# Performance work log

Hardware: AMD Instinct MI355X
Metric: run time of the kernel (lower is better)

## Reference

```python
import jax, jax.numpy as jnp
import numpy as np

B, T, C = 2, 2048, 1024
H = 16
DH = C // H  # 64
EPS = 1e-5


def setup_inputs() -> dict:
    key = jax.random.key(0)
    ks = jax.random.split(key, 12)
    s = lambda k, shape, fan: jax.random.normal(k, shape, jnp.float32) / np.sqrt(fan)
    return {
        'x': jax.random.normal(ks[0], (B, T, C), jnp.float32),
        'wq': s(ks[1], (H, C, DH), C),
        'wk': s(ks[2], (H, C, DH), C),
        'wv': s(ks[3], (H, C, DH), C),
        'w_proj': s(ks[4], (C, C), C),
        'b_proj': jnp.zeros((C,), jnp.float32),
        'g_ln1': jnp.ones((C,), jnp.float32),
        'b_ln1': jnp.zeros((C,), jnp.float32),
        'g_ln2': jnp.ones((C,), jnp.float32),
        'b_ln2': jnp.zeros((C,), jnp.float32),
        'w_ff1': s(ks[5], (C, 4 * C), C),
        'b_ff1': jnp.zeros((4 * C,), jnp.float32),
        'w_ff2': s(ks[6], (4 * C, C), 4 * C),
        'b_ff2': jnp.zeros((C,), jnp.float32),
    }


def _layernorm(x, g, b):
    mu = jnp.mean(x, axis=-1, keepdims=True)
    var = jnp.mean(jnp.square(x - mu), axis=-1, keepdims=True)
    return (x - mu) * jax.lax.rsqrt(var + EPS) * g + b


def _attention(x, wq, wk, wv, w_proj, b_proj):
    # per-head projections, batched over heads: [B,T,C] x [H,C,Dh] -> [B,H,T,Dh]
    q = jnp.einsum('btc,hcd->bhtd', x, wq)
    k = jnp.einsum('btc,hcd->bhtd', x, wk)
    v = jnp.einsum('btc,hcd->bhtd', x, wv)
    scores = jnp.einsum('bhtd,bhsd->bhts', q, k) / np.sqrt(DH).astype(np.float32)
    t = x.shape[1]
    causal = jnp.tril(jnp.ones((t, t), bool))
    scores = jnp.where(causal, scores, -jnp.inf)
    w = jax.nn.softmax(scores, axis=-1)
    out = jnp.einsum('bhts,bhsd->bhtd', w, v)  # [B,H,T,Dh]
    # concat heads (head order matches torch cat over head list)
    out = out.transpose(0, 2, 1, 3).reshape(x.shape[0], t, C)
    return out @ w_proj + b_proj


def reference(x, wq, wk, wv, w_proj, b_proj, g_ln1, b_ln1, g_ln2, b_ln2, w_ff1, b_ff1, w_ff2, b_ff2):
    x = x + _attention(_layernorm(x, g_ln1, b_ln1), wq, wk, wv, w_proj, b_proj)
    h = _layernorm(x, g_ln2, b_ln2)
    ff = jax.nn.relu(h @ w_ff1 + b_ff1) @ w_ff2 + b_ff2
    return x + ff
```

## Files before the change

### kernel.cpp

```cpp
#include <hip/hip_runtime.h>

#define DEV __device__ __forceinline__

typedef __attribute__((ext_vector_type(4))) float f32x4;
typedef __attribute__((ext_vector_type(8))) short short8;
typedef __attribute__((ext_vector_type(8))) __bf16 bf16x8;

DEV unsigned short f2bf(float f) {
  __bf16 h = (__bf16)f;
  return __builtin_bit_cast(unsigned short, h);
}
DEV unsigned pack2(float a, float b) {
  return (unsigned)f2bf(a) | ((unsigned)f2bf(b) << 16);
}
DEV bf16x8 ld_bf8(const unsigned short* p) {
  short8 v = *(const short8*)p;
  return __builtin_bit_cast(bf16x8, v);
}
DEV f32x4 MFMA(bf16x8 a, bf16x8 b, f32x4 c) {
  return __builtin_amdgcn_mfma_f32_16x16x32_bf16(a, b, c, 0, 0, 0);
}

typedef const __attribute__((address_space(1))) void GV;
typedef __attribute__((address_space(3))) void LV;
DEV void gl_lds16(const void* g, void* l) {
  __builtin_amdgcn_global_load_lds((GV*)g, (LV*)l, 16, 0, 0);
}

DEV void xcd_decode(int gx, int& bx, int& by) {
  const int nwg = gridDim.x, bid = blockIdx.x;
  const int cpx = nwg >> 3;
  const int swz = (bid & 7) * cpx + (bid >> 3);
  by = swz / gx;
  bx = swz % gx;
}

__global__ void __launch_bounds__(256) ln_fused(
    const float* __restrict__ x, const float* __restrict__ g,
    const float* __restrict__ b, unsigned short* __restrict__ y)
{
  const int row = blockIdx.x, tid = threadIdx.x;
  const float4 xv = ((const float4*)(x + (size_t)row * 1024))[tid];
  float s  = xv.x + xv.y + xv.z + xv.w;
  float s2 = xv.x * xv.x + xv.y * xv.y + xv.z * xv.z + xv.w * xv.w;
#pragma unroll
  for (int o = 32; o > 0; o >>= 1) { s += __shfl_down(s, o); s2 += __shfl_down(s2, o); }
  __shared__ float ps[4], ps2[4];
  if ((tid & 63) == 0) { ps[tid >> 6] = s; ps2[tid >> 6] = s2; }
  __syncthreads();
  float S  = ps[0] + ps[1] + ps[2] + ps[3];
  float S2 = ps2[0] + ps2[1] + ps2[2] + ps2[3];
  float mu = S * (1.f / 1024.f);
  float rs = rsqrtf(S2 * (1.f / 1024.f) - mu * mu + 1e-5f);
  const float4 gv = ((const float4*)g)[tid];
  const float4 bv = ((const float4*)b)[tid];
  uint2 r;
  r.x = pack2((xv.x - mu) * rs * gv.x + bv.x, (xv.y - mu) * rs * gv.y + bv.y);
  r.y = pack2((xv.z - mu) * rs * gv.z + bv.z, (xv.w - mu) * rs * gv.w + bv.w);
  ((uint2*)(y + (size_t)row * 1024))[tid] = r;
}

__global__ void __launch_bounds__(256) transp_f2b(
    const float* __restrict__ src, unsigned short* __restrict__ dst, int R, int C)
{
  __shared__ float t[64][65];
  const int c0 = blockIdx.x * 64, r0 = blockIdx.y * 64;
  const int tx = threadIdx.x & 63, tq = threadIdx.x >> 6;
#pragma unroll
  for (int i = 0; i < 16; i++) {
    int r = tq * 16 + i;
    t[r][tx] = src[(size_t)(r0 + r) * C + c0 + tx];
  }
  __syncthreads();
#pragma unroll
  for (int i = 0; i < 16; i++) {
    int c = tq * 16 + i;
    dst[(size_t)(c0 + c) * R + r0 + tx] = f2bf(t[tx][c]);
  }
}

__global__ void __launch_bounds__(256) qkv_transp(
    const float* __restrict__ wq, const float* __restrict__ wk,
    const float* __restrict__ wv, unsigned short* __restrict__ dst)
{
  __shared__ float t[64][65];
  const int c0 = blockIdx.x * 64, h = blockIdx.y, z = blockIdx.z;
  const float* w = (z == 0 ? wq : z == 1 ? wk : wv) + (size_t)h * 1024 * 64;
  const int tx = threadIdx.x & 63, tq = threadIdx.x >> 6;
#pragma unroll
  for (int i = 0; i < 16; i++) {
    int c = tq * 16 + i;
    t[c][tx] = w[(size_t)(c0 + c) * 64 + tx];
  }
  __syncthreads();
  unsigned short* drow = dst + (size_t)(z * 1024 + h * 64) * 1024 + c0;
#pragma unroll
  for (int i = 0; i < 16; i++) {
    int d = tq * 16 + i;
    drow[(size_t)d * 1024 + tx] = f2bf(t[tx][d]);
  }
}

__global__ void __launch_bounds__(256) v_transp(
    const unsigned short* __restrict__ qkv, unsigned short* __restrict__ vt)
{
  __shared__ unsigned s[64][65];
  const int t0 = blockIdx.x * 64, h = blockIdx.y, b = blockIdx.z;
  const int tx = threadIdx.x & 63, tq = threadIdx.x >> 6;
#pragma unroll
  for (int i = 0; i < 16; i++) {
    int tr = tq * 16 + i;
    s[tr][tx] = qkv[(size_t)(b * 2048 + t0 + tr) * 3072 + 2048 + h * 64 + tx];
  }
  __syncthreads();
  unsigned short* vb = vt + (size_t)((b * 16 + h) * 64) * 2048 + t0;
#pragma unroll
  for (int i = 0; i < 16; i++) {
    int d = tq * 16 + i;
    vb[(size_t)d * 2048 + tx] = (unsigned short)s[tx][d];
  }
}

template<int BIAS, int RELU, int RES, int OBF>
__global__ void __launch_bounds__(256) gemm_bt(
    const unsigned short* __restrict__ A, const unsigned short* __restrict__ Bt,
    const float* __restrict__ bias, const float* __restrict__ res,
    void* __restrict__ out, int M, int N, int K, int gx)
{
  __shared__ unsigned short As[2][128 * 32];
  __shared__ unsigned short Bs[2][128 * 32];
  int bx, by;
  xcd_decode(gx, bx, by);
  const int tid = threadIdx.x;
  const int wid = tid >> 6, lane = tid & 63;
  const int lg = lane >> 4, lr = lane & 15;
  const int m0 = by * 128, n0 = bx * 128;
  const int wr = (wid >> 1) * 64, wc = (wid & 1) * 64;

  const int srow = tid >> 2;
  const int scs = (tid & 3) ^ (srow & 3);
  const unsigned short* ga = A + (size_t)(m0 + srow) * K + scs * 8;
  const unsigned short* gb = Bt + (size_t)(n0 + srow) * K + scs * 8;
  const int ca = (lg ^ (lr & 3)) * 8;

  f32x4 acc[4][4] = {};

  auto stage = [&](int buf, int k0) {
    char* asb = (char*)&As[buf][0] + wid * 1024;
    char* bsb = (char*)&Bs[buf][0] + wid * 1024;
    gl_lds16(ga + k0, asb);
    gl_lds16(ga + k0 + (size_t)64 * K, asb + 4096);
    gl_lds16(gb + k0, bsb);
    gl_lds16(gb + k0 + (size_t)64 * K, bsb + 4096);
  };

  stage(0, 0);
  int cur = 0;
  for (int k0 = 0; k0 < K; k0 += 32) {
    __syncthreads();
    if (k0 + 32 < K) stage(cur ^ 1, k0 + 32);
    bf16x8 a[4], b[4];
#pragma unroll
    for (int m = 0; m < 4; m++) a[m] = ld_bf8(&As[cur][(wr + m * 16 + lr) * 32 + ca]);
#pragma unroll
    for (int n = 0; n < 4; n++) b[n] = ld_bf8(&Bs[cur][(wc + n * 16 + lr) * 32 + ca]);
#pragma unroll
    for (int m = 0; m < 4; m++)
#pragma unroll
      for (int n = 0; n < 4; n++)
        acc[m][n] = MFMA(a[m], b[n], acc[m][n]);
    cur ^= 1;
  }

#pragma unroll
  for (int m = 0; m < 4; m++) {
    const int row0 = m0 + wr + m * 16 + lg * 4;
#pragma unroll
    for (int n = 0; n < 4; n++) {
      const int col = n0 + wc + n * 16 + lr;
      const float bv = BIAS ? bias[col] : 0.f;
#pragma unroll
      for (int r = 0; r < 4; r++) {
        const size_t off = (size_t)(row0 + r) * N + col;
        float v = acc[m][n][r] + bv;
        if (RES) v += res[off];
        if (RELU) v = v > 0.f ? v : 0.f;
        if (OBF) ((unsigned short*)out)[off] = f2bf(v);
        else     ((float*)out)[off] = v;
      }
    }
  }
}

template<int BIAS, int RELU, int RES, int OBF>
__global__ void __launch_bounds__(256) gemm_bt64(
    const unsigned short* __restrict__ A, const unsigned short* __restrict__ Bt,
    const float* __restrict__ bias, const float* __restrict__ res,
    void* __restrict__ out, int M, int N, int K, int gx)
{
  __shared__ unsigned short As[2][64 * 64];
  __shared__ unsigned short Bs[2][128 * 64];
  int bx, by;
  xcd_decode(gx, bx, by);
  const int tid = threadIdx.x;
  const int wid = tid >> 6, lane = tid & 63;
  const int lg = lane >> 4, lr = lane & 15;
  const int m0 = by * 64, n0 = bx * 128;
  const int wr = (wid >> 1) * 32, wc = (wid & 1) * 64;

  const int srow = tid >> 3;
  const int scs = (tid & 7) ^ (srow & 7);
  const unsigned short* ga = A + (size_t)(m0 + srow) * K + scs * 8;
  const unsigned short* gb = Bt + (size_t)(n0 + srow) * K + scs * 8;
  const int lxs = lr & 7;

  f32x4 acc[2][4] = {};

  auto stage = [&](int buf, int k0) {
    char* asb = (char*)&As[buf][0] + wid * 1024;
    char* bsb = (char*)&Bs[buf][0] + wid * 1024;
    gl_lds16(ga + k0, asb);
    gl_lds16(ga + k0 + (size_t)32 * K, asb + 4096);
    gl_lds16(gb + k0, bsb);
    gl_lds16(gb + k0 + (size_t)32 * K, bsb + 4096);
    gl_lds16(gb + k0 + (size_t)64 * K, bsb + 8192);
    gl_lds16(gb + k0 + (size_t)96 * K, bsb + 12288);
  };

  stage(0, 0);
  int cur = 0;
  for (int k0 = 0; k0 < K; k0 += 64) {
    __syncthreads();
    if (k0 + 64 < K) stage(cur ^ 1, k0 + 64);
#pragma unroll
    for (int kk = 0; kk < 2; kk++) {
      const int cb = kk * 4;
      bf16x8 a[2], b[4];
#pragma unroll
      for (int m = 0; m < 2; m++)
        a[m] = ld_bf8(&As[cur][(wr + m * 16 + lr) * 64 + ((cb + lg) ^ lxs) * 8]);
#pragma unroll
      for (int n = 0; n < 4; n++)
        b[n] = ld_bf8(&Bs[cur][(wc + n * 16 + lr) * 64 + ((cb + lg) ^ lxs) * 8]);
#pragma unroll
      for (int m = 0; m < 2; m++)
#pragma unroll
        for (int n = 0; n < 4; n++)
          acc[m][n] = MFMA(a[m], b[n], acc[m][n]);
    }
    cur ^= 1;
  }

#pragma unroll
  for (int m = 0; m < 2; m++) {
    const int row0 = m0 + wr + m * 16 + lg * 4;
#pragma unroll
    for (int n = 0; n < 4; n++) {
      const int col = n0 + wc + n * 16 + lr;
      const float bv = BIAS ? bias[col] : 0.f;
#pragma unroll
      for (int r = 0; r < 4; r++) {
        const size_t off = (size_t)(row0 + r) * N + col;
        float v = acc[m][n][r] + bv;
        if (RES) v += res[off];
        if (RELU) v = v > 0.f ? v : 0.f;
        if (OBF) ((unsigned short*)out)[off] = f2bf(v);
        else     ((float*)out)[off] = v;
      }
    }
  }
}

__global__ void __launch_bounds__(256) attn_fwd(
    const unsigned short* __restrict__ qkv, const unsigned short* __restrict__ vt,
    unsigned short* __restrict__ out)
{
  __shared__ unsigned short Ks[2][64 * 64];
  __shared__ unsigned short Vs[2][64 * 64];
  __shared__ unsigned short P[4][16][72];

  int j, bh;
  xcd_decode(16, j, bh);
  const int b = bh >> 4, h = bh & 15;
  const int tid = threadIdx.x, wid = tid >> 6, lane = tid & 63;
  const int lg = lane >> 4, lr = lane & 15;

  const int tA = j, tB = 31 - j;
  const int nkt = tB + 1;
  const float C2 = 0.18033688f;
  const float THRRAW = 44.3614f;

  const unsigned short* kbase = qkv + (size_t)(b * 2048) * 3072 + 1024 + h * 64;
  const unsigned short* vbase = vt + (size_t)(bh * 64) * 2048;

  const int sr = tid >> 3;
  const int sc = tid & 7;
  const int c0 = sc ^ (sr & 7);

  auto stage = [&](int buf, int kt) {
    const int kv0 = kt * 64;
    char* kd = (char*)&Ks[buf][0] + wid * 1024;
    char* vd = (char*)&Vs[buf][0] + wid * 1024;
    gl_lds16(kbase + (size_t)(kv0 + sr) * 3072 + c0 * 8, kd);
    gl_lds16(kbase + (size_t)(kv0 + 32 + sr) * 3072 + c0 * 8, kd + 4096);
    gl_lds16(vbase + (size_t)sr * 2048 + kv0 + c0 * 8, vd);
    gl_lds16(vbase + (size_t)(32 + sr) * 2048 + kv0 + c0 * 8, vd + 4096);
  };

  auto process = [&](int kt, int qt, const bf16x8& qf0, const bf16x8& qf1,
                     f32x4 (&o)[4], float& m, float& l, int buf) {
    const int kv0 = kt * 64;
    const int qg = qt * 64 + wid * 16 + lr;
    const unsigned short* Kb = &Ks[buf][0];
    const unsigned short* Vb = &Vs[buf][0];
    f32x4 s[4] = {};
    __builtin_amdgcn_s_setprio(1);
#pragma unroll
    for (int f = 0; f < 4; f++) {
      const int row = f * 16 + lr;
      const int rc = row & 7;
      s[f] = MFMA(ld_bf8(Kb + row * 64 + (lg ^ rc) * 8), qf0, s[f]);
      s[f] = MFMA(ld_bf8(Kb + row * 64 + ((lg | 4) ^ rc) * 8), qf1, s[f]);
    }
    __builtin_amdgcn_s_setprio(0);
    float p[16];
    float mt = -1e30f;
    const bool diag = (kt == qt);
#pragma unroll
    for (int f = 0; f < 4; f++)
#pragma unroll
      for (int r = 0; r < 4; r++) {
        float sv = s[f][r];
        if (diag) {
          const int kv = kv0 + f * 16 + lg * 4 + r;
          sv = (kv <= qg) ? sv : -1e30f;
        }
        p[f * 4 + r] = sv;
        mt = fmaxf(mt, sv);
      }
    mt = fmaxf(mt, __shfl_xor(mt, 16));
    mt = fmaxf(mt, __shfl_xor(mt, 32));
    if (!__all(mt - m <= THRRAW)) {
      const float mnew = fmaxf(m, mt);
      const float sf = exp2f(C2 * (m - mnew));
      l *= sf;
#pragma unroll
      for (int df = 0; df < 4; df++) o[df] *= sf;
      m = mnew;
    }
    const float cm = C2 * m;
    float ps = 0.f;
#pragma unroll
    for (int i = 0; i < 16; i++) {
      p[i] = exp2f(fmaf(p[i], C2, -cm));
      ps += p[i];
    }
    ps += __shfl_xor(ps, 16);
    ps += __shfl_xor(ps, 32);
    l += ps;
    unsigned short* Pr = &P[wid][lr][0];
#pragma unroll
    for (int f = 0; f < 4; f++) {
      *(unsigned*)(Pr + f * 16 + lg * 4)     = pack2(p[f * 4 + 0], p[f * 4 + 1]);
      *(unsigned*)(Pr + f * 16 + lg * 4 + 2) = pack2(p[f * 4 + 2], p[f * 4 + 3]);
    }
    const bf16x8 pf0 = ld_bf8(Pr + lg * 8);
    const bf16x8 pf1 = ld_bf8(Pr + 32 + lg * 8);
    __builtin_amdgcn_s_setprio(1);
#pragma unroll
    for (int df = 0; df < 4; df++) {
      const int row = df * 16 + lr;
      const int rc = row & 7;
      o[df] = MFMA(ld_bf8(Vb + row * 64 + (lg ^ rc) * 8), pf0, o[df]);
      o[df] = MFMA(ld_bf8(Vb + row * 64 + ((lg | 4) ^ rc) * 8), pf1, o[df]);
    }
    __builtin_amdgcn_s_setprio(0);
  };

  const unsigned short* qb = qkv + (size_t)(b * 2048) * 3072 + h * 64;
  const int qrA = tA * 64 + wid * 16 + lr;
  const int qrB = tB * 64 + wid * 16 + lr;
  const bf16x8 qA0 = ld_bf8(qb + (size_t)qrA * 3072 + lg * 8);
  const bf16x8 qA1 = ld_bf8(qb + (size_t)qrA * 3072 + 32 + lg * 8);
  const bf16x8 qB0 = ld_bf8(qb + (size_t)qrB * 3072 + lg * 8);
  const bf16x8 qB1 = ld_bf8(qb + (size_t)qrB * 3072 + 32 + lg * 8);

  f32x4 oA[4] = {}, oB[4] = {};
  float mA = -1e30f, lA = 0.f, mB = -1e30f, lB = 0.f;

  stage(0, 0);
  __syncthreads();
  for (int kt = 0; kt < nkt; kt++) {
    const int buf = kt & 1;
    if (kt + 1 < nkt) stage(buf ^ 1, kt + 1);
    if (kt <= tA) process(kt, tA, qA0, qA1, oA, mA, lA, buf);
    process(kt, tB, qB0, qB1, oB, mB, lB, buf);
    __syncthreads();
  }

  const float invA = 1.f / lA, invB = 1.f / lB;
  {
    const int qg = tA * 64 + wid * 16 + lr;
    unsigned* orow = (unsigned*)(out + (size_t)(b * 2048 + qg) * 1024 + h * 64 + lg * 4);
#pragma unroll
    for (int df = 0; df < 4; df++) {
      orow[df * 8 + 0] = pack2(oA[df][0] * invA, oA[df][1] * invA);
      orow[df * 8 + 1] = pack2(oA[df][2] * invA, oA[df][3] * invA);
    }
  }
  {
    const int qg = tB * 64 + wid * 16 + lr;
    unsigned* orow = (unsigned*)(out + (size_t)(b * 2048 + qg) * 1024 + h * 64 + lg * 4);
#pragma unroll
    for (int df = 0; df < 4; df++) {
      orow[df * 8 + 0] = pack2(oB[df][0] * invB, oB[df][1] * invB);
      orow[df * 8 + 1] = pack2(oB[df][2] * invB, oB[df][3] * invB);
    }
  }
}

extern "C" void kernel_launch(void* const* d_in, const int* in_sizes, int n_in,
                              void* d_out, int out_size, void* d_ws, size_t ws_size,
                              hipStream_t stream)
{
  const float* x     = (const float*)d_in[0];
  const float* wq    = (const float*)d_in[1];
  const float* wk    = (const float*)d_in[2];
  const float* wv    = (const float*)d_in[3];
  const float* wproj = (const float*)d_in[4];
  const float* bproj = (const float*)d_in[5];
  const float* gln1  = (const float*)d_in[6];
  const float* bln1  = (const float*)d_in[7];
  const float* gln2  = (const float*)d_in[8];
  const float* bln2  = (const float*)d_in[9];
  const float* wff1  = (const float*)d_in[10];
  const float* bff1  = (const float*)d_in[11];
  const float* wff2  = (const float*)d_in[12];
  const float* bff2  = (const float*)d_in[13];

  char* ws = (char*)d_ws;
  const size_t MB = 1u << 20;
  float*          x2    = (float*)         (ws + 0 * MB);
  unsigned short* hbuf  = (unsigned short*)(ws + 16 * MB);
  unsigned short* xn1   = (unsigned short*)(ws + 24 * MB);
  unsigned short* attn  = (unsigned short*)(ws + 24 * MB);
  unsigned short* qkvb  = (unsigned short*)(ws + 32 * MB);
  unsigned short* vtb   = (unsigned short*)(ws + 56 * MB);
  unsigned short* a1    = (unsigned short*)(ws + 32 * MB);
  unsigned short* wqkvT = (unsigned short*)(ws + 64 * MB);
  unsigned short* wprojT= (unsigned short*)(ws + 70 * MB);
  unsigned short* wff1T = (unsigned short*)(ws + 72 * MB);
  unsigned short* wff2T = (unsigned short*)(ws + 80 * MB);

  qkv_transp<<<dim3(16, 16, 3), 256, 0, stream>>>(wq, wk, wv, wqkvT);
  transp_f2b<<<dim3(16, 16), 256, 0, stream>>>(wproj, wprojT, 1024, 1024);
  transp_f2b<<<dim3(64, 16), 256, 0, stream>>>(wff1, wff1T, 1024, 4096);
  transp_f2b<<<dim3(16, 64), 256, 0, stream>>>(wff2, wff2T, 4096, 1024);

  ln_fused<<<4096, 256, 0, stream>>>(x, gln1, bln1, xn1);
  gemm_bt<0, 0, 0, 1><<<768, 256, 0, stream>>>(
      xn1, wqkvT, nullptr, nullptr, qkvb, 4096, 3072, 1024, 24);
  v_transp<<<dim3(32, 16, 2), 256, 0, stream>>>(qkvb, vtb);
  attn_fwd<<<512, 256, 0, stream>>>(qkvb, vtb, attn);
  gemm_bt64<1, 0, 1, 0><<<512, 256, 0, stream>>>(
      attn, wprojT, bproj, x, x2, 4096, 1024, 1024, 8);
  ln_fused<<<4096, 256, 0, stream>>>(x2, gln2, bln2, hbuf);
  gemm_bt<1, 1, 0, 1><<<1024, 256, 0, stream>>>(
      hbuf, wff1T, bff1, nullptr, a1, 4096, 4096, 1024, 32);
  gemm_bt64<1, 0, 1, 0><<<512, 256, 0, stream>>>(
      a1, wff2T, bff2, x2, (float*)d_out, 4096, 1024, 4096, 8);
}
```

Measured before the change: 253.0 us.

## Split attention into one query tile per block and shrink N-narrow GEMM tiles

The attention kernel no longer pairs two query tiles per block for causal load balancing. It now launches 1024 blocks, each handling one query tile, with a swizzled block index that schedules the longest tiles first. The two narrow-N GEMMs (output projection and FFN2) use 64x64 tiles instead of 64x128, doubling the block count. The aim is more blocks in flight on the many CUs, at the cost of less data reuse per block and uneven per-block work in attention.

Result: slower. 259.9 us (+2.7%).

```diff
diff --git a/kernel.cpp b/kernel.cpp
--- a/kernel.cpp
+++ b/kernel.cpp
@@ -193,20 +193,20 @@
 }
 
 template<int BIAS, int RELU, int RES, int OBF>
-__global__ void __launch_bounds__(256) gemm_bt64(
+__global__ void __launch_bounds__(256) gemm_64(
     const unsigned short* __restrict__ A, const unsigned short* __restrict__ Bt,
     const float* __restrict__ bias, const float* __restrict__ res,
     void* __restrict__ out, int M, int N, int K, int gx)
 {
   __shared__ unsigned short As[2][64 * 64];
-  __shared__ unsigned short Bs[2][128 * 64];
+  __shared__ unsigned short Bs[2][64 * 64];
   int bx, by;
   xcd_decode(gx, bx, by);
   const int tid = threadIdx.x;
   const int wid = tid >> 6, lane = tid & 63;
   const int lg = lane >> 4, lr = lane & 15;
-  const int m0 = by * 64, n0 = bx * 128;
-  const int wr = (wid >> 1) * 32, wc = (wid & 1) * 64;
+  const int m0 = by * 64, n0 = bx * 64;
+  const int wr = (wid >> 1) * 32, wc = (wid & 1) * 32;
 
   const int srow = tid >> 3;
   const int scs = (tid & 7) ^ (srow & 7);
@@ -214,7 +214,7 @@
   const unsigned short* gb = Bt + (size_t)(n0 + srow) * K + scs * 8;
   const int lxs = lr & 7;
 
-  f32x4 acc[2][4] = {};
+  f32x4 acc[2][2] = {};
 
   auto stage = [&](int buf, int k0) {
     char* asb = (char*)&As[buf][0] + wid * 1024;
@@ -223,8 +223,6 @@
     gl_lds16(ga + k0 + (size_t)32 * K, asb + 4096);
     gl_lds16(gb + k0, bsb);
     gl_lds16(gb + k0 + (size_t)32 * K, bsb + 4096);
-    gl_lds16(gb + k0 + (size_t)64 * K, bsb + 8192);
-    gl_lds16(gb + k0 + (size_t)96 * K, bsb + 12288);
   };
 
   stage(0, 0);
@@ -235,17 +233,17 @@
 #pragma unroll
     for (int kk = 0; kk < 2; kk++) {
       const int cb = kk * 4;
-      bf16x8 a[2], b[4];
+      bf16x8 a[2], b[2];
 #pragma unroll
       for (int m = 0; m < 2; m++)
         a[m] = ld_bf8(&As[cur][(wr + m * 16 + lr) * 64 + ((cb + lg) ^ lxs) * 8]);
 #pragma unroll
-      for (int n = 0; n < 4; n++)
+      for (int n = 0; n < 2; n++)
         b[n] = ld_bf8(&Bs[cur][(wc + n * 16 + lr) * 64 + ((cb + lg) ^ lxs) * 8]);
 #pragma unroll
       for (int m = 0; m < 2; m++)
 #pragma unroll
-        for (int n = 0; n < 4; n++)
+        for (int n = 0; n < 2; n++)
           acc[m][n] = MFMA(a[m], b[n], acc[m][n]);
     }
     cur ^= 1;
@@ -255,7 +253,7 @@
   for (int m = 0; m < 2; m++) {
     const int row0 = m0 + wr + m * 16 + lg * 4;
 #pragma unroll
-    for (int n = 0; n < 4; n++) {
+    for (int n = 0; n < 2; n++) {
       const int col = n0 + wc + n * 16 + lr;
       const float bv = BIAS ? bias[col] : 0.f;
 #pragma unroll
@@ -279,14 +277,15 @@
   __shared__ unsigned short Vs[2][64 * 64];
   __shared__ unsigned short P[4][16][72];
 
-  int j, bh;
-  xcd_decode(16, j, bh);
+  const int bid = blockIdx.x;
+  const int swz = (bid & 7) * 128 + (bid >> 3);
+  const int bh = swz >> 5;
+  const int qt = 31 - (swz & 31);
   const int b = bh >> 4, h = bh & 15;
   const int tid = threadIdx.x, wid = tid >> 6, lane = tid & 63;
   const int lg = lane >> 4, lr = lane & 15;
 
-  const int tA = j, tB = 31 - j;
-  const int nkt = tB + 1;
+  const int nkt = qt + 1;
   const float C2 = 0.18033688f;
   const float THRRAW = 44.3614f;
 
@@ -307,10 +306,21 @@
     gl_lds16(vbase + (size_t)(32 + sr) * 2048 + kv0 + c0 * 8, vd + 4096);
   };
 
-  auto process = [&](int kt, int qt, const bf16x8& qf0, const bf16x8& qf1,
-                     f32x4 (&o)[4], float& m, float& l, int buf) {
+  const unsigned short* qb = qkv + (size_t)(b * 2048) * 3072 + h * 64;
+  const int qg = qt * 64 + wid * 16 + lr;
+  const bf16x8 qf0 = ld_bf8(qb + (size_t)qg * 3072 + lg * 8);
+  const bf16x8 qf1 = ld_bf8(qb + (size_t)qg * 3072 + 32 + lg * 8);
+
+  f32x4 o[4] = {};
+  float m = -1e30f, l = 0.f;
+
+  stage(0, 0);
+  __syncthreads();
+  for (int kt = 0; kt < nkt; kt++) {
+    const int buf = kt & 1;
+    if (kt + 1 < nkt) stage(buf ^ 1, kt + 1);
+
     const int kv0 = kt * 64;
-    const int qg = qt * 64 + wid * 16 + lr;
     const unsigned short* Kb = &Ks[buf][0];
     const unsigned short* Vb = &Vs[buf][0];
     f32x4 s[4] = {};
@@ -375,47 +385,15 @@
       o[df] = MFMA(ld_bf8(Vb + row * 64 + ((lg | 4) ^ rc) * 8), pf1, o[df]);
     }
     __builtin_amdgcn_s_setprio(0);
-  };
-
-  const unsigned short* qb = qkv + (size_t)(b * 2048) * 3072 + h * 64;
-  const int qrA = tA * 64 + wid * 16 + lr;
-  const int qrB = tB * 64 + wid * 16 + lr;
-  const bf16x8 qA0 = ld_bf8(qb + (size_t)qrA * 3072 + lg * 8);
-  const bf16x8 qA1 = ld_bf8(qb + (size_t)qrA * 3072 + 32 + lg * 8);
-  const bf16x8 qB0 = ld_bf8(qb + (size_t)qrB * 3072 + lg * 8);
-  const bf16x8 qB1 = ld_bf8(qb + (size_t)qrB * 3072 + 32 + lg * 8);
-
-  f32x4 oA[4] = {}, oB[4] = {};
-  float mA = -1e30f, lA = 0.f, mB = -1e30f, lB = 0.f;
-
-  stage(0, 0);
-  __syncthreads();
-  for (int kt = 0; kt < nkt; kt++) {
-    const int buf = kt & 1;
-    if (kt + 1 < nkt) stage(buf ^ 1, kt + 1);
-    if (kt <= tA) process(kt, tA, qA0, qA1, oA, mA, lA, buf);
-    process(kt, tB, qB0, qB1, oB, mB, lB, buf);
     __syncthreads();
   }
 
-  const float invA = 1.f / lA, invB = 1.f / lB;
-  {
-    const int qg = tA * 64 + wid * 16 + lr;
-    unsigned* orow = (unsigned*)(out + (size_t)(b * 2048 + qg) * 1024 + h * 64 + lg * 4);
-#pragma unroll
-    for (int df = 0; df < 4; df++) {
-      orow[df * 8 + 0] = pack2(oA[df][0] * invA, oA[df][1] * invA);
-      orow[df * 8 + 1] = pack2(oA[df][2] * invA, oA[df][3] * invA);
-    }
-  }
-  {
-    const int qg = tB * 64 + wid * 16 + lr;
-    unsigned* orow = (unsigned*)(out + (size_t)(b * 2048 + qg) * 1024 + h * 64 + lg * 4);
-#pragma unroll
-    for (int df = 0; df < 4; df++) {
-      orow[df * 8 + 0] = pack2(oB[df][0] * invB, oB[df][1] * invB);
-      orow[df * 8 + 1] = pack2(oB[df][2] * invB, oB[df][3] * invB);
-    }
+  const float inv = 1.f / l;
+  unsigned* orow = (unsigned*)(out + (size_t)(b * 2048 + qg) * 1024 + h * 64 + lg * 4);
+#pragma unroll
+  for (int df = 0; df < 4; df++) {
+    orow[df * 8 + 0] = pack2(o[df][0] * inv, o[df][1] * inv);
+    orow[df * 8 + 1] = pack2(o[df][2] * inv, o[df][3] * inv);
   }
 }
 
@@ -461,12 +439,12 @@
   gemm_bt<0, 0, 0, 1><<<768, 256, 0, stream>>>(
       xn1, wqkvT, nullptr, nullptr, qkvb, 4096, 3072, 1024, 24);
   v_transp<<<dim3(32, 16, 2), 256, 0, stream>>>(qkvb, vtb);
-  attn_fwd<<<512, 256, 0, stream>>>(qkvb, vtb, attn);
-  gemm_bt64<1, 0, 1, 0><<<512, 256, 0, stream>>>(
-      attn, wprojT, bproj, x, x2, 4096, 1024, 1024, 8);
+  attn_fwd<<<1024, 256, 0, stream>>>(qkvb, vtb, attn);
+  gemm_64<1, 0, 1, 0><<<1024, 256, 0, stream>>>(
+      attn, wprojT, bproj, x, x2, 4096, 1024, 1024, 16);
   ln_fused<<<4096, 256, 0, stream>>>(x2, gln2, bln2, hbuf);
   gemm_bt<1, 1, 0, 1><<<1024, 256, 0, stream>>>(
       hbuf, wff1T, bff1, nullptr, a1, 4096, 4096, 1024, 32);
-  gemm_bt64<1, 0, 1, 0><<<512, 256, 0, stream>>>(
-      a1, wff2T, bff2, x2, (float*)d_out, 4096, 1024, 4096, 8);
-}
+  gemm_64<1, 0, 1, 0><<<1024, 256, 0, stream>>>(
+      a1, wff2T, bff2, x2, (float*)d_out, 4096, 1024, 4096, 16);
+}
```

## Use 64x64 GEMM tiles for N=1024 projections and stage 128 KV rows in attention

Applied to the files above, without the earlier changes.

The N=1024 GEMMs (output projection and FF2) switch from 64x128 to 64x64 tiles, doubling the grid to 1024 blocks so the GPU's CUs are better filled. Separately, the attention kernel now stages K/V in 128-row chunks and processes two 64-row tiles per barrier, halving the number of synchronisations per KV sweep. The trade-offs are lower per-block operand reuse in the GEMMs and twice the K/V shared memory in attention, which can reduce occupancy.

After: 247.1 us. -2.3%, faster.

```diff
diff --git a/kernel.cpp b/kernel.cpp
--- a/kernel.cpp
+++ b/kernel.cpp
@@ -193,20 +193,20 @@
 }
 
 template<int BIAS, int RELU, int RES, int OBF>
-__global__ void __launch_bounds__(256) gemm_bt64(
+__global__ void __launch_bounds__(256) gemm_64(
     const unsigned short* __restrict__ A, const unsigned short* __restrict__ Bt,
     const float* __restrict__ bias, const float* __restrict__ res,
     void* __restrict__ out, int M, int N, int K, int gx)
 {
   __shared__ unsigned short As[2][64 * 64];
-  __shared__ unsigned short Bs[2][128 * 64];
+  __shared__ unsigned short Bs[2][64 * 64];
   int bx, by;
   xcd_decode(gx, bx, by);
   const int tid = threadIdx.x;
   const int wid = tid >> 6, lane = tid & 63;
   const int lg = lane >> 4, lr = lane & 15;
-  const int m0 = by * 64, n0 = bx * 128;
-  const int wr = (wid >> 1) * 32, wc = (wid & 1) * 64;
+  const int m0 = by * 64, n0 = bx * 64;
+  const int wr = (wid >> 1) * 32, wc = (wid & 1) * 32;
 
   const int srow = tid >> 3;
   const int scs = (tid & 7) ^ (srow & 7);
@@ -214,7 +214,7 @@
   const unsigned short* gb = Bt + (size_t)(n0 + srow) * K + scs * 8;
   const int lxs = lr & 7;
 
-  f32x4 acc[2][4] = {};
+  f32x4 acc[2][2] = {};
 
   auto stage = [&](int buf, int k0) {
     char* asb = (char*)&As[buf][0] + wid * 1024;
@@ -223,8 +223,6 @@
     gl_lds16(ga + k0 + (size_t)32 * K, asb + 4096);
     gl_lds16(gb + k0, bsb);
     gl_lds16(gb + k0 + (size_t)32 * K, bsb + 4096);
-    gl_lds16(gb + k0 + (size_t)64 * K, bsb + 8192);
-    gl_lds16(gb + k0 + (size_t)96 * K, bsb + 12288);
   };
 
   stage(0, 0);
@@ -235,17 +233,17 @@
 #pragma unroll
     for (int kk = 0; kk < 2; kk++) {
       const int cb = kk * 4;
-      bf16x8 a[2], b[4];
+      bf16x8 a[2], b[2];
 #pragma unroll
       for (int m = 0; m < 2; m++)
         a[m] = ld_bf8(&As[cur][(wr + m * 16 + lr) * 64 + ((cb + lg) ^ lxs) * 8]);
 #pragma unroll
-      for (int n = 0; n < 4; n++)
+      for (int n = 0; n < 2; n++)
         b[n] = ld_bf8(&Bs[cur][(wc + n * 16 + lr) * 64 + ((cb + lg) ^ lxs) * 8]);
 #pragma unroll
       for (int m = 0; m < 2; m++)
 #pragma unroll
-        for (int n = 0; n < 4; n++)
+        for (int n = 0; n < 2; n++)
           acc[m][n] = MFMA(a[m], b[n], acc[m][n]);
     }
     cur ^= 1;
@@ -255,7 +253,7 @@
   for (int m = 0; m < 2; m++) {
     const int row0 = m0 + wr + m * 16 + lg * 4;
 #pragma unroll
-    for (int n = 0; n < 4; n++) {
+    for (int n = 0; n < 2; n++) {
       const int col = n0 + wc + n * 16 + lr;
       const float bv = BIAS ? bias[col] : 0.f;
 #pragma unroll
@@ -275,8 +273,8 @@
     const unsigned short* __restrict__ qkv, const unsigned short* __restrict__ vt,
     unsigned short* __restrict__ out)
 {
-  __shared__ unsigned short Ks[2][64 * 64];
-  __shared__ unsigned short Vs[2][64 * 64];
+  __shared__ unsigned short Ks[2][128 * 64];
+  __shared__ unsigned short Vs[2][128 * 64];
   __shared__ unsigned short P[4][16][72];
 
   int j, bh;
@@ -287,6 +285,7 @@
 
   const int tA = j, tB = 31 - j;
   const int nkt = tB + 1;
+  const int npair = (nkt + 1) >> 1;
   const float C2 = 0.18033688f;
   const float THRRAW = 44.3614f;
 
@@ -297,22 +296,26 @@
   const int sc = tid & 7;
   const int c0 = sc ^ (sr & 7);
 
-  auto stage = [&](int buf, int kt) {
-    const int kv0 = kt * 64;
+  auto stage = [&](int buf, int p) {
+    const int kv0 = p * 128;
     char* kd = (char*)&Ks[buf][0] + wid * 1024;
     char* vd = (char*)&Vs[buf][0] + wid * 1024;
     gl_lds16(kbase + (size_t)(kv0 + sr) * 3072 + c0 * 8, kd);
     gl_lds16(kbase + (size_t)(kv0 + 32 + sr) * 3072 + c0 * 8, kd + 4096);
+    gl_lds16(kbase + (size_t)(kv0 + 64 + sr) * 3072 + c0 * 8, kd + 8192);
+    gl_lds16(kbase + (size_t)(kv0 + 96 + sr) * 3072 + c0 * 8, kd + 12288);
     gl_lds16(vbase + (size_t)sr * 2048 + kv0 + c0 * 8, vd);
     gl_lds16(vbase + (size_t)(32 + sr) * 2048 + kv0 + c0 * 8, vd + 4096);
+    gl_lds16(vbase + (size_t)sr * 2048 + kv0 + 64 + c0 * 8, vd + 8192);
+    gl_lds16(vbase + (size_t)(32 + sr) * 2048 + kv0 + 64 + c0 * 8, vd + 12288);
   };
 
   auto process = [&](int kt, int qt, const bf16x8& qf0, const bf16x8& qf1,
                      f32x4 (&o)[4], float& m, float& l, int buf) {
     const int kv0 = kt * 64;
     const int qg = qt * 64 + wid * 16 + lr;
-    const unsigned short* Kb = &Ks[buf][0];
-    const unsigned short* Vb = &Vs[buf][0];
+    const unsigned short* Kb = &Ks[buf][(kt & 1) << 12];
+    const unsigned short* Vb = &Vs[buf][(kt & 1) << 12];
     f32x4 s[4] = {};
     __builtin_amdgcn_s_setprio(1);
 #pragma unroll
@@ -390,11 +393,14 @@
 
   stage(0, 0);
   __syncthreads();
-  for (int kt = 0; kt < nkt; kt++) {
-    const int buf = kt & 1;
-    if (kt + 1 < nkt) stage(buf ^ 1, kt + 1);
-    if (kt <= tA) process(kt, tA, qA0, qA1, oA, mA, lA, buf);
-    process(kt, tB, qB0, qB1, oB, mB, lB, buf);
+  for (int p = 0; p < npair; p++) {
+    const int buf = p & 1;
+    if (p + 1 < npair) stage(buf ^ 1, p + 1);
+    const int kt0 = 2 * p, kt1 = 2 * p + 1;
+    if (kt0 <= tA) process(kt0, tA, qA0, qA1, oA, mA, lA, buf);
+    if (kt1 <= tA) process(kt1, tA, qA0, qA1, oA, mA, lA, buf);
+    process(kt0, tB, qB0, qB1, oB, mB, lB, buf);
+    if (kt1 < nkt) process(kt1, tB, qB0, qB1, oB, mB, lB, buf);
     __syncthreads();
   }
 
@@ -462,11 +468,11 @@
       xn1, wqkvT, nullptr, nullptr, qkvb, 4096, 3072, 1024, 24);
   v_transp<<<dim3(32, 16, 2), 256, 0, stream>>>(qkvb, vtb);
   attn_fwd<<<512, 256, 0, stream>>>(qkvb, vtb, attn);
-  gemm_bt64<1, 0, 1, 0><<<512, 256, 0, stream>>>(
-      attn, wprojT, bproj, x, x2, 4096, 1024, 1024, 8);
+  gemm_64<1, 0, 1, 0><<<1024, 256, 0, stream>>>(
+      attn, wprojT, bproj, x, x2, 4096, 1024, 1024, 16);
   ln_fused<<<4096, 256, 0, stream>>>(x2, gln2, bln2, hbuf);
   gemm_bt<1, 1, 0, 1><<<1024, 256, 0, stream>>>(
       hbuf, wff1T, bff1, nullptr, a1, 4096, 4096, 1024, 32);
-  gemm_bt64<1, 0, 1, 0><<<512, 256, 0, stream>>>(
-      a1, wff2T, bff2, x2, (float*)d_out, 4096, 1024, 4096, 8);
-}
+  gemm_64<1, 0, 1, 0><<<1024, 256, 0, stream>>>(
+      a1, wff2T, bff2, x2, (float*)d_out, 4096, 1024, 4096, 16);
+}
```
